# Optimization experiments

Hardware: AMD Instinct MI355X
Metric: run time of the kernel (lower is better)

The kernel has to match this reference:

```python
import jax, jax.numpy as jnp
import numpy as np

EPS = 1e-6      # eps used in token2map / map2token weight normalization
LN_EPS = 1e-5   # torch nn.LayerNorm default


def layernorm(x, w, b):
    m = jnp.mean(x, axis=-1, keepdims=True)
    xc = x - m
    v = jnp.mean(xc * xc, axis=-1, keepdims=True)
    return xc * jax.lax.rsqrt(v + LN_EPS) * w + b


def grid_index(H_init, W_init, H, W):
    # nearest-neighbor map: flattened feature-map index for each init-grid cell
    r = (jnp.arange(H_init) * H) // H_init
    c = (jnp.arange(W_init) * W) // W_init
    return (r[:, None] * W + c[None, :]).reshape(-1)  # [N_init]


def token2map(x, idx_token, H, W, H_init, W_init):
    # tokens [B,N,C] -> feature map [B,H,W,C] via weighted scatter-mean
    B, N, C = x.shape
    idx_hw = grid_index(H_init, W_init, H, W)                    # [N_init]
    counts = jnp.zeros((H * W,), x.dtype).at[idx_hw].add(1.0)    # identical across batch
    w = (1.0 / (counts + EPS))[idx_hw]                           # [N_init]
    src = jnp.take_along_axis(x, idx_token[..., None], axis=1)   # [B,N_init,C]
    out = jnp.zeros((B, H * W, C), x.dtype).at[:, idx_hw, :].add(src * w[None, :, None])
    return out.reshape(B, H, W, C)


def map2token(fmap, idx_token, N, H_init, W_init):
    # feature map [B,H,W,C] -> tokens [B,N,C]: mean of member grid cells per token
    B, H, W, C = fmap.shape
    idx_hw = grid_index(H_init, W_init, H, W)
    bidx = jnp.arange(B)[:, None]
    counts = jnp.zeros((B, N), fmap.dtype).at[bidx, idx_token].add(1.0)
    wt = jnp.take_along_axis(1.0 / (counts + EPS), idx_token, axis=1)  # [B,N_init]
    src = fmap.reshape(B, H * W, C)[:, idx_hw, :]                      # [B,N_init,C]
    return jnp.zeros((B, N, C), fmap.dtype).at[bidx, idx_token].add(src * wt[..., None])


def _forward(x, token_score, idx_token,
             norm1_w, norm1_b, q_w, q_b, kv_w, kv_b, sr_w, sr_b, srn_w, srn_b,
             proj_w, proj_b, norm2_w, norm2_b, fc1_w, fc1_b, skip_w, dw_w, dw_b,
             fc2_w, fc2_b, H, W, H_init, W_init, token_num, num_heads):
    B, N, C = x.shape
    d = C // num_heads
    scale = d ** -0.5
    sr = 2  # sr_ratio

    xn = layernorm(x, norm1_w, norm1_b)  # q_dict['x'] = norm1(x); kv_dict is q_dict

    # ---- TCFormerDynamicAttention ----
    q = (xn @ q_w + q_b).reshape(B, N, num_heads, d).transpose(0, 2, 1, 3)  # [B,h,N,d]
    tmp = jnp.concatenate([xn, token_score], axis=-1)            # [B,N,C+1]
    tmp_map = token2map(tmp, idx_token, H, W, H_init, W_init)    # [B,H,W,C+1]
    kv_map, conf_map = tmp_map[..., :C], tmp_map[..., C]
    kv = jax.lax.conv_general_dilated(kv_map, sr_w, (sr, sr), 'VALID',
        dimension_numbers=('NHWC', 'HWIO', 'NHWC')) + sr_b       # sr conv, stride 2
    M = (H // sr) * (W // sr)
    kv = layernorm(kv.reshape(B, M, C), srn_w, srn_b)
    conf = conf_map.reshape(B, H // sr, sr, W // sr, sr).mean(axis=(2, 4)).reshape(B, M)

    kv = (kv @ kv_w + kv_b).reshape(B, M, 2, num_heads, d)
    k = kv[:, :, 0].transpose(0, 2, 1, 3)                        # [B,h,M,d]
    v = kv[:, :, 1].transpose(0, 2, 1, 3)
    attn = jnp.einsum('bhnd,bhmd->bhnm', q * scale, k) + conf[:, None, None, :]
    attn = jax.nn.softmax(attn, axis=-1)
    a = jnp.einsum('bhnm,bhmd->bhnd', attn, v).transpose(0, 2, 1, 3).reshape(B, N, C)
    x = x + (a @ proj_w + proj_b)

    # ---- TCMLP ----
    h = layernorm(x, norm2_w, norm2_b) @ fc1_w + fc1_b           # [B,N,H1]
    hmap = token2map(h, idx_token, H, W, H_init, W_init)         # [B,H,W,H1]
    hmap = jax.lax.conv_general_dilated(hmap, dw_w, (1, 1), ((1, 1), (1, 1)),
        dimension_numbers=('NHWC', 'HWIO', 'NHWC'),
        feature_group_count=h.shape[-1]) + dw_b                  # depthwise 3x3
    hc = h * skip_w + map2token(hmap, idx_token, N, H_init, W_init)  # skip = dw 1x1 conv1d
    hc = jax.nn.gelu(hc, approximate=False)
    return x + (hc @ fc2_w + fc2_b)


def setup_inputs() -> dict:
    B, N, C, H1 = 8, 1568, 256, 1024
    H = W = 56
    H_init = W_init = 112
    key = jax.random.key(0)
    ks = jax.random.split(key, 16)
    r = lambda i, shape, s=0.02: jax.random.normal(ks[i], shape, jnp.float32) * s
    return {
        'x': jax.random.normal(ks[0], (B, N, C), jnp.float32),
        'token_score': jax.random.normal(ks[1], (B, N, 1), jnp.float32),
        'idx_token': jax.random.randint(ks[2], (B, H_init * W_init), 0, N),
        'norm1_w': jnp.ones((C,), jnp.float32), 'norm1_b': jnp.zeros((C,), jnp.float32),
        'q_w': r(3, (C, C)), 'q_b': jnp.zeros((C,), jnp.float32),
        'kv_w': r(4, (C, 2 * C)), 'kv_b': jnp.zeros((2 * C,), jnp.float32),
        'sr_w': r(5, (2, 2, C, C)), 'sr_b': jnp.zeros((C,), jnp.float32),
        'srn_w': jnp.ones((C,), jnp.float32), 'srn_b': jnp.zeros((C,), jnp.float32),
        'proj_w': r(6, (C, C)), 'proj_b': jnp.zeros((C,), jnp.float32),
        'norm2_w': jnp.ones((C,), jnp.float32), 'norm2_b': jnp.zeros((C,), jnp.float32),
        'fc1_w': r(7, (C, H1)), 'fc1_b': jnp.zeros((H1,), jnp.float32),
        'skip_w': 1.0 + r(8, (H1,), 0.1),
        'dw_w': r(9, (3, 3, 1, H1), 0.1), 'dw_b': jnp.zeros((H1,), jnp.float32),
        'fc2_w': r(10, (H1, C)), 'fc2_b': jnp.zeros((C,), jnp.float32),
        'H': H, 'W': W, 'H_init': H_init, 'W_init': W_init,
        'token_num': N, 'num_heads': 8,
    }


def reference(x, token_score, idx_token, norm1_w, norm1_b, q_w, q_b, kv_w, kv_b,
              sr_w, sr_b, srn_w, srn_b, proj_w, proj_b, norm2_w, norm2_b,
              fc1_w, fc1_b, skip_w, dw_w, dw_b, fc2_w, fc2_b,
              H, W, H_init, W_init, token_num, num_heads):
    return _forward(x, token_score, idx_token, norm1_w, norm1_b, q_w, q_b, kv_w, kv_b,
                    sr_w, sr_b, srn_w, srn_b, proj_w, proj_b, norm2_w, norm2_b,
                    fc1_w, fc1_b, skip_w, dw_w, dw_b, fc2_w, fc2_b,
                    H, W, H_init, W_init, token_num, num_heads)
```

## Files before the change

kernel.cpp:

```cpp
#include <hip/hip_runtime.h>
#include <math.h>

#define BB 8
#define NTOK 1568
#define CD 256
#define HIMG 56
#define WIMG 56
#define HWSZ 3136
#define HIG 112
#define WIG 112
#define NI 12544
#define MKV 784
#define MPAD 800
#define NHEADS 8
#define HEADD 32
#define HH1 1024
#define ROWS1 (BB*NTOK)
#define ROWSK (BB*MKV)
#define LOG2E 1.4426950408889634f

typedef unsigned short bfu;
typedef __attribute__((ext_vector_type(4))) unsigned short bf4;
typedef __attribute__((ext_vector_type(8))) unsigned short bf8;
typedef __attribute__((ext_vector_type(8))) short s8v;
typedef __attribute__((ext_vector_type(16))) float f16v;

__device__ inline float b2f(bfu u) { union { unsigned i; float f; } x; x.i = (unsigned)u << 16; return x.f; }
__device__ inline bfu f2b(float f) {
  union { float f; unsigned i; } x; x.f = f;
  unsigned r = x.i + 0x7fffu + ((x.i >> 16) & 1u);
  return (bfu)(r >> 16);
}
__device__ inline int get_isb(const unsigned* probe) { return probe[0] == 0x3F803F80u ? 1 : 0; }
__device__ inline float ldd(const void* p, size_t i, int isb) {
  return isb ? b2f(((const bfu*)p)[i]) : ((const float*)p)[i];
}
__device__ inline int xswz(int wg, int nwg) {
  return (nwg & 7) ? wg : (wg & 7) * (nwg >> 3) + (wg >> 3);
}

__global__ __launch_bounds__(256) void wtr_tile(const void* __restrict__ w0,
                                                const void* __restrict__ w1,
                                                const void* __restrict__ w2,
                                                const void* __restrict__ w3,
                                                const void* __restrict__ w4,
                                                const void* __restrict__ w5,
                                                const void* __restrict__ w6,
                                                const void* __restrict__ w7,
                                                bfu* __restrict__ wtb,
                                                const unsigned* __restrict__ probe) {
  int isb = get_isb(probe);
  int bid = blockIdx.x, tid = threadIdx.x;
  if (bid >= 1024) {
    int idx = (bid - 1024) * 256 + tid;
    if (idx < 9216) wtb[1048576 + idx] = f2b(ldd(w6, idx, isb));
    else            wtb[1048576 + idx] = f2b(ldd(w7, idx - 9216, isb));
    return;
  }
  const void* W; int K, N; bfu* Wt; int tloc;
  if (bid < 64)       { W = w0; K = 256;  N = 256;  Wt = wtb;          tloc = bid; }
  else if (bid < 320) { W = w1; K = 1024; N = 256;  Wt = wtb + 65536;  tloc = bid - 64; }
  else if (bid < 448) { W = w2; K = 256;  N = 512;  Wt = wtb + 327680; tloc = bid - 320; }
  else if (bid < 512) { W = w3; K = 256;  N = 256;  Wt = wtb + 458752; tloc = bid - 448; }
  else if (bid < 768) { W = w4; K = 256;  N = 1024; Wt = wtb + 524288; tloc = bid - 512; }
  else                { W = w5; K = 1024; N = 256;  Wt = wtb + 786432; tloc = bid - 768; }
  int ntn = N >> 5;
  int tn = tloc % ntn, tk = tloc / ntn;
  int n0 = tn * 32, k0 = tk * 32;
  __shared__ float s[32][33];
  int tx = tid & 31, ty = tid >> 5;
#pragma unroll
  for (int i = 0; i < 4; i++) {
    int k = ty + 8 * i;
    s[k][tx] = ldd(W, (size_t)(k0 + k) * N + n0 + tx, isb);
  }
  __syncthreads();
#pragma unroll
  for (int i = 0; i < 4; i++) {
    int n = ty + 8 * i;
    Wt[(size_t)(n0 + n) * K + k0 + tx] = f2b(s[tx][n]);
  }
}

__global__ __launch_bounds__(256) void ln_kernel(const void* __restrict__ in, int inmode,
                                                 const void* __restrict__ w,
                                                 const void* __restrict__ bta,
                                                 bfu* __restrict__ out,
                                                 const unsigned* __restrict__ probe) {
  int isb = get_isb(probe);
  int im = (inmode == 2) ? isb : inmode;
  int blk = xswz(blockIdx.x, gridDim.x);
  int wv = threadIdx.x >> 6, lane = threadIdx.x & 63;
  int row = blk * 4 + wv;
  int c4 = lane * 4;
  float v[4];
  if (im) {
    bf4 t = *(const bf4*)((const bfu*)in + (size_t)row * CD + c4);
#pragma unroll
    for (int j = 0; j < 4; j++) v[j] = b2f(t[j]);
  } else {
    float4 t = *(const float4*)((const float*)in + (size_t)row * CD + c4);
    v[0] = t.x; v[1] = t.y; v[2] = t.z; v[3] = t.w;
  }
  float s1 = v[0] + v[1] + v[2] + v[3];
  float s2 = v[0] * v[0] + v[1] * v[1] + v[2] * v[2] + v[3] * v[3];
#pragma unroll
  for (int off = 1; off < 64; off <<= 1) {
    s1 += __shfl_xor(s1, off);
    s2 += __shfl_xor(s2, off);
  }
  float m = s1 * (1.0f / CD);
  float inv = rsqrtf(s2 * (1.0f / CD) - m * m + 1e-5f);
  bf4 ov;
#pragma unroll
  for (int j = 0; j < 4; j++)
    ov[j] = f2b((v[j] - m) * inv * ldd(w, c4 + j, isb) + ldd(bta, c4 + j, isb));
  *(bf4*)(out + (size_t)row * CD + c4) = ov;
}

__global__ __launch_bounds__(256) void rgemm(const bfu* __restrict__ A,
                                             const bfu* __restrict__ Bt,
                                             const void* __restrict__ bias,
                                             const void* __restrict__ resid, int rmode,
                                             void* __restrict__ Cc, int cmode,
                                             void* __restrict__ aux,
                                             int K, int Ncols,
                                             const unsigned* __restrict__ probe) {
  int isb = get_isb(probe);
  int rm = (rmode == 1) ? (isb ? 3 : 2) : rmode;
  int cm = (cmode == 2) ? (isb ? 0 : 1) : cmode;
  int nbx = Ncols >> 6;
  int id = xswz(blockIdx.x, gridDim.x);
  int bx = id % nbx, by = id / nbx;
  int w = threadIdx.x >> 6, lane = threadIdx.x & 63;
  int l31 = lane & 31, hi = lane >> 5;
  int m0 = by * 128 + w * 32;
  int c0 = bx * 64;
  const bfu* pa  = A  + (size_t)(m0 + l31) * K + hi * 8;
  const bfu* pb0 = Bt + (size_t)(c0 + l31) * K + hi * 8;
  const bfu* pb1 = Bt + (size_t)(c0 + 32 + l31) * K + hi * 8;
  f16v acc0, acc1;
#pragma unroll
  for (int r = 0; r < 16; r++) { acc0[r] = 0.f; acc1[r] = 0.f; }
  s8v aA  = *(const s8v*)(pa),       b0A = *(const s8v*)(pb0),      b1A = *(const s8v*)(pb1);
  s8v aB  = *(const s8v*)(pa + 16),  b0B = *(const s8v*)(pb0 + 16), b1B = *(const s8v*)(pb1 + 16);
  for (int k0 = 32; k0 <= K; k0 += 32) {
    s8v caA = aA, cb0A = b0A, cb1A = b1A, caB = aB, cb0B = b0B, cb1B = b1B;
    if (k0 < K) {
      aA  = *(const s8v*)(pa + k0);       b0A = *(const s8v*)(pb0 + k0);      b1A = *(const s8v*)(pb1 + k0);
      aB  = *(const s8v*)(pa + k0 + 16);  b0B = *(const s8v*)(pb0 + k0 + 16); b1B = *(const s8v*)(pb1 + k0 + 16);
    }
    __builtin_amdgcn_s_setprio(1);
    acc0 = __builtin_amdgcn_mfma_f32_32x32x16_bf16(caA, cb0A, acc0, 0, 0, 0);
    acc1 = __builtin_amdgcn_mfma_f32_32x32x16_bf16(caA, cb1A, acc1, 0, 0, 0);
    acc0 = __builtin_amdgcn_mfma_f32_32x32x16_bf16(caB, cb0B, acc0, 0, 0, 0);
    acc1 = __builtin_amdgcn_mfma_f32_32x32x16_bf16(caB, cb1B, acc1, 0, 0, 0);
    __builtin_amdgcn_s_setprio(0);
  }
  float bw0 = ldd(bias, c0 + l31, isb);
  float bw1 = ldd(bias, c0 + 32 + l31, isb);
#pragma unroll
  for (int r = 0; r < 16; r++) {
    int row = m0 + (r & 3) + 8 * (r >> 2) + 4 * hi;
    size_t base0 = (size_t)row * Ncols + c0 + l31;
    size_t base1 = base0 + 32;
    float v0 = acc0[r] + bw0;
    float v1 = acc1[r] + bw1;
    if (rm == 2) { v0 += ((const float*)resid)[base0]; v1 += ((const float*)resid)[base1]; }
    else if (rm == 3) { v0 += b2f(((const bfu*)resid)[base0]); v1 += b2f(((const bfu*)resid)[base1]); }
    if (cm == 0) { ((bfu*)Cc)[base0] = f2b(v0); ((bfu*)Cc)[base1] = f2b(v1); }
    else if (cm == 1) { ((float*)Cc)[base0] = v0; ((float*)Cc)[base1] = v1; }
    else {
      int bb = row / MKV, mm = row - bb * MKV;
      int col0c = c0 + l31;
      if (col0c < 256) ((bfu*)Cc)[base0] = f2b(v0);
      else ((bfu*)aux)[((size_t)(bb * 256) + (col0c - 256)) * MPAD + mm] = f2b(v0);
      int col1c = col0c + 32;
      if (col1c < 256) ((bfu*)Cc)[base1] = f2b(v1);
      else ((bfu*)aux)[((size_t)(bb * 256) + (col1c - 256)) * MPAD + mm] = f2b(v1);
    }
  }
}

__global__ __launch_bounds__(256) void akv_kernel(const bfu* __restrict__ xn,
                                                  const void* __restrict__ tscore,
                                                  const int* __restrict__ idx_token,
                                                  bfu* __restrict__ Akv,
                                                  float* __restrict__ conf,
                                                  const unsigned* __restrict__ probe) {
  int isb = get_isb(probe);
  int blk = xswz(blockIdx.x, gridDim.x), tid = threadIdx.x;
  int b = blk / MKV, m = blk % MKV;
  int i2 = m / 28, j2 = m % 28;
  __shared__ int nn[16];
  __shared__ float cacc[16];
  if (tid < 16) {
    int a = (tid >> 3) & 1, kb = (tid >> 2) & 1, di = (tid >> 1) & 1, dj = tid & 1;
    int ti = 4 * i2 + 2 * a + di, tj = 4 * j2 + 2 * kb + dj;
    int n = idx_token[b * NI + ti * WIG + tj];
    nn[tid] = n;
    cacc[tid] = ldd(tscore, b * NTOK + n, isb);
  }
  __syncthreads();
  const float w4 = 1.0f / (4.0f + 1e-6f);
  int g = tid >> 6, c4 = (tid & 63) * 4;
  bf4 a0 = *(const bf4*)(xn + (size_t)(b * NTOK + nn[g * 4 + 0]) * CD + c4);
  bf4 a1 = *(const bf4*)(xn + (size_t)(b * NTOK + nn[g * 4 + 1]) * CD + c4);
  bf4 a2 = *(const bf4*)(xn + (size_t)(b * NTOK + nn[g * 4 + 2]) * CD + c4);
  bf4 a3 = *(const bf4*)(xn + (size_t)(b * NTOK + nn[g * 4 + 3]) * CD + c4);
  bf4 rv;
#pragma unroll
  for (int j = 0; j < 4; j++)
    rv[j] = f2b(w4 * (b2f(a0[j]) + b2f(a1[j]) + b2f(a2[j]) + b2f(a3[j])));
  *(bf4*)(Akv + (size_t)blk * 1024 + g * CD + c4) = rv;
  if (tid == 0) {
    float s = 0.f;
    for (int k = 0; k < 16; k++) s += cacc[k];
    conf[b * MPAD + m] = 0.25f * w4 * s * 5.656854249492381f;
  }
}

__global__ __launch_bounds__(256) void pad_kernel(bfu* __restrict__ vt, float* __restrict__ conf) {
  int t = blockIdx.x * 256 + threadIdx.x;
  int b = t / 4096, rem = t % 4096;
  int d = rem / 16, m = MKV + (rem % 16);
  vt[((size_t)(b * 256 + d)) * MPAD + m] = 0;
  if (t < 128) conf[(t / 16) * MPAD + MKV + (t % 16)] = -1e30f;
}

__global__ __launch_bounds__(256) void attn_kernel(const bfu* __restrict__ qb,
                                                   const bfu* __restrict__ kv,
                                                   const bfu* __restrict__ vt,
                                                   const float* __restrict__ conf,
                                                   bfu* __restrict__ out) {
  __shared__ float sdata[4][64][34];
  int tid = threadIdx.x;
  int w = tid >> 6, lane = tid & 63;
  int l31 = lane & 31, hi = lane >> 5;
  int blk = xswz(blockIdx.x, gridDim.x);
  int qt = blk % 25, tt = blk / 25;
  int hh = tt & 7, b = tt >> 3;
  int n0 = qt * 64;
  int two = (qt < 24);
  const bfu* qrow1 = qb + (size_t)(b * NTOK + n0 + l31) * CD + hh * HEADD + hi * 8;
  s8v qfA1 = *(const s8v*)(qrow1);
  s8v qfB1 = *(const s8v*)(qrow1 + 16);
  s8v qfA2 = {0, 0, 0, 0, 0, 0, 0, 0}, qfB2 = qfA2;
  if (two) {
    const bfu* qrow2 = qrow1 + (size_t)32 * CD;
    qfA2 = *(const s8v*)(qrow2);
    qfB2 = *(const s8v*)(qrow2 + 16);
  }
  const float scale = 0.17677669529663689f * LOG2E;
  const bfu* kbase = kv + hh * HEADD + hi * 8;
  const bfu* vbase = vt + ((size_t)(b * 256 + hh * HEADD + l31)) * MPAD + hi * 8;
  const float* cbase = conf + b * MPAD + 4 * hi;
  f16v oc1, oc2;
#pragma unroll
  for (int r = 0; r < 16; r++) { oc1[r] = 0.f; oc2[r] = 0.f; }
  float lr1 = 0.f, lr2 = 0.f;
  int w32 = w * 32;
  const bfu* kp0 = kbase + (size_t)(b * MKV + w32 + l31) * 512;
  s8v kfA = *(const s8v*)(kp0);
  s8v kfB = *(const s8v*)(kp0 + 16);
  s8v vfA = *(const s8v*)(vbase + w32);
  s8v vfB = *(const s8v*)(vbase + w32 + 16);
  float4 cf0 = *(const float4*)(cbase + w32);
  float4 cf1 = *(const float4*)(cbase + w32 + 8);
  float4 cf2 = *(const float4*)(cbase + w32 + 16);
  float4 cf3 = *(const float4*)(cbase + w32 + 24);
  for (int m0 = w32; m0 < MPAD; m0 += 128) {
    s8v ckA = kfA, ckB = kfB, cvA = vfA, cvB = vfB;
    float4 d0 = cf0, d1 = cf1, d2 = cf2, d3 = cf3;
    int m1 = m0 + 128;
    if (m1 < MPAD) {
      int mA = m1 + l31; if (mA > MKV - 1) mA = MKV - 1;
      const bfu* kp = kbase + (size_t)(b * MKV + mA) * 512;
      kfA = *(const s8v*)(kp);
      kfB = *(const s8v*)(kp + 16);
      vfA = *(const s8v*)(vbase + m1);
      vfB = *(const s8v*)(vbase + m1 + 16);
      cf0 = *(const float4*)(cbase + m1);
      cf1 = *(const float4*)(cbase + m1 + 8);
      cf2 = *(const float4*)(cbase + m1 + 16);
      cf3 = *(const float4*)(cbase + m1 + 24);
    }
    f16v cseed;
    cseed[0] = d0.x; cseed[1] = d0.y; cseed[2] = d0.z; cseed[3] = d0.w;
    cseed[4] = d1.x; cseed[5] = d1.y; cseed[6] = d1.z; cseed[7] = d1.w;
    cseed[8] = d2.x; cseed[9] = d2.y; cseed[10] = d2.z; cseed[11] = d2.w;
    cseed[12] = d3.x; cseed[13] = d3.y; cseed[14] = d3.z; cseed[15] = d3.w;
    __builtin_amdgcn_s_setprio(1);
    f16v c = __builtin_amdgcn_mfma_f32_32x32x16_bf16(ckA, qfA1, cseed, 0, 0, 0);
    c = __builtin_amdgcn_mfma_f32_32x32x16_bf16(ckB, qfB1, c, 0, 0, 0);
    __builtin_amdgcn_s_setprio(0);
    {
      float p[16], ps0 = 0.f, ps1 = 0.f, ps2 = 0.f, ps3 = 0.f;
#pragma unroll
      for (int r = 0; r < 16; r++) {
        p[r] = __builtin_amdgcn_exp2f(c[r] * scale);
        if ((r & 3) == 0) ps0 += p[r];
        else if ((r & 3) == 1) ps1 += p[r];
        else if ((r & 3) == 2) ps2 += p[r];
        else ps3 += p[r];
      }
      lr1 += (ps0 + ps1) + (ps2 + ps3);
      unsigned Z[8];
#pragma unroll
      for (int a2 = 0; a2 < 8; a2++)
        asm("v_cvt_pk_bf16_f32 %0, %1, %2" : "=v"(Z[a2]) : "v"(p[2 * a2]), "v"(p[2 * a2 + 1]));
      asm("v_permlane32_swap_b32 %0, %1" : "+v"(Z[0]), "+v"(Z[2]));
      asm("v_permlane32_swap_b32 %0, %1" : "+v"(Z[1]), "+v"(Z[3]));
      asm("v_permlane32_swap_b32 %0, %1" : "+v"(Z[4]), "+v"(Z[6]));
      asm("v_permlane32_swap_b32 %0, %1" : "+v"(Z[5]), "+v"(Z[7]));
      union { unsigned u[4]; s8v v; } B1, B2;
      B1.u[0] = Z[0]; B1.u[1] = Z[1]; B1.u[2] = Z[2]; B1.u[3] = Z[3];
      B2.u[0] = Z[4]; B2.u[1] = Z[5]; B2.u[2] = Z[6]; B2.u[3] = Z[7];
      __builtin_amdgcn_s_setprio(1);
      oc1 = __builtin_amdgcn_mfma_f32_32x32x16_bf16(cvA, B1.v, oc1, 0, 0, 0);
      oc1 = __builtin_amdgcn_mfma_f32_32x32x16_bf16(cvB, B2.v, oc1, 0, 0, 0);
      __builtin_amdgcn_s_setprio(0);
    }
    if (two) {
      __builtin_amdgcn_s_setprio(1);
      f16v c2 = __builtin_amdgcn_mfma_f32_32x32x16_bf16(ckA, qfA2, cseed, 0, 0, 0);
      c2 = __builtin_amdgcn_mfma_f32_32x32x16_bf16(ckB, qfB2, c2, 0, 0, 0);
      __builtin_amdgcn_s_setprio(0);
      float p[16], ps0 = 0.f, ps1 = 0.f, ps2 = 0.f, ps3 = 0.f;
#pragma unroll
      for (int r = 0; r < 16; r++) {
        p[r] = __builtin_amdgcn_exp2f(c2[r] * scale);
        if ((r & 3) == 0) ps0 += p[r];
        else if ((r & 3) == 1) ps1 += p[r];
        else if ((r & 3) == 2) ps2 += p[r];
        else ps3 += p[r];
      }
      lr2 += (ps0 + ps1) + (ps2 + ps3);
      unsigned Z[8];
#pragma unroll
      for (int a2 = 0; a2 < 8; a2++)
        asm("v_cvt_pk_bf16_f32 %0, %1, %2" : "=v"(Z[a2]) : "v"(p[2 * a2]), "v"(p[2 * a2 + 1]));
      asm("v_permlane32_swap_b32 %0, %1" : "+v"(Z[0]), "+v"(Z[2]));
      asm("v_permlane32_swap_b32 %0, %1" : "+v"(Z[1]), "+v"(Z[3]));
      asm("v_permlane32_swap_b32 %0, %1" : "+v"(Z[4]), "+v"(Z[6]));
      asm("v_permlane32_swap_b32 %0, %1" : "+v"(Z[5]), "+v"(Z[7]));
      union { unsigned u[4]; s8v v; } B1, B2;
      B1.u[0] = Z[0]; B1.u[1] = Z[1]; B1.u[2] = Z[2]; B1.u[3] = Z[3];
      B2.u[0] = Z[4]; B2.u[1] = Z[5]; B2.u[2] = Z[6]; B2.u[3] = Z[7];
      __builtin_amdgcn_s_setprio(1);
      oc2 = __builtin_amdgcn_mfma_f32_32x32x16_bf16(cvA, B1.v, oc2, 0, 0, 0);
      oc2 = __builtin_amdgcn_mfma_f32_32x32x16_bf16(cvB, B2.v, oc2, 0, 0, 0);
      __builtin_amdgcn_s_setprio(0);
    }
  }
#pragma unroll
  for (int r = 0; r < 16; r++) { sdata[w][lane][r] = oc1[r]; sdata[w][lane][17 + r] = oc2[r]; }
  sdata[w][lane][16] = lr1;
  sdata[w][lane][33] = lr2;
  __syncthreads();
  if (w == 0 || (w == 1 && two)) {
    int base = w * 17;
    float s[17];
#pragma unroll
    for (int r = 0; r < 17; r++)
      s[r] = sdata[0][lane][base + r] + sdata[1][lane][base + r] +
             sdata[2][lane][base + r] + sdata[3][lane][base + r];
    float l = s[16];
    l += __shfl_xor(l, 32);
    float inv = 1.0f / l;
    bfu* op = out + (size_t)(b * NTOK + n0 + w * 32 + l31) * CD + hh * HEADD + 4 * hi;
#pragma unroll
    for (int g = 0; g < 4; g++) {
      bf4 o;
#pragma unroll
      for (int u = 0; u < 4; u++) o[u] = f2b(s[4 * g + u] * inv);
      *(bf4*)(op + 8 * g) = o;
    }
  }
}

__global__ __launch_bounds__(128) void hmap_kernel(const bfu* __restrict__ h,
                                                   const int* __restrict__ idx_token,
                                                   bfu* __restrict__ hmap) {
  int blk = xswz(blockIdx.x, gridDim.x), tid = threadIdx.x;
  int b = blk / HWSZ, cell = blk % HWSZ;
  int i = cell / WIMG, j = cell % WIMG;
  __shared__ int nn[4];
  if (tid < 4) {
    int di = tid >> 1, dj = tid & 1;
    nn[tid] = idx_token[b * NI + (2 * i + di) * WIG + (2 * j + dj)];
  }
  __syncthreads();
  const float w4 = 1.0f / (4.0f + 1e-6f);
  int c8 = tid * 8;
  bf8 a0 = *(const bf8*)(h + (size_t)(b * NTOK + nn[0]) * HH1 + c8);
  bf8 a1 = *(const bf8*)(h + (size_t)(b * NTOK + nn[1]) * HH1 + c8);
  bf8 a2 = *(const bf8*)(h + (size_t)(b * NTOK + nn[2]) * HH1 + c8);
  bf8 a3 = *(const bf8*)(h + (size_t)(b * NTOK + nn[3]) * HH1 + c8);
  bf8 rv;
#pragma unroll
  for (int j2 = 0; j2 < 8; j2++)
    rv[j2] = f2b(w4 * (b2f(a0[j2]) + b2f(a1[j2]) + b2f(a2[j2]) + b2f(a3[j2])));
  *(bf8*)(hmap + (size_t)blk * HH1 + c8) = rv;
}

__global__ __launch_bounds__(256) void dw_kernel(const bfu* __restrict__ hmap,
                                                 const bfu* __restrict__ dwt,
                                                 const bfu* __restrict__ dbt,
                                                 bfu* __restrict__ dwout) {
  int blk = xswz(blockIdx.x, gridDim.x);
  int j4 = blk % 14; int rem = blk / 14;
  int i = rem % HIMG; int b = rem / HIMG;
  int tid = threadIdx.x;
  int c4 = tid * 4;
  int j0 = j4 * 4;
  float wf[9][4];
#pragma unroll
  for (int k = 0; k < 9; k++) {
    bf4 wv = *(const bf4*)(dwt + k * HH1 + c4);
#pragma unroll
    for (int u = 0; u < 4; u++) wf[k][u] = b2f(wv[u]);
  }
  bf4 bias = *(const bf4*)(dbt + c4);
  float bi[4];
#pragma unroll
  for (int u = 0; u < 4; u++) bi[u] = b2f(bias[u]);
  bf4 tp[3][6];
  const size_t bbase = (size_t)b * HWSZ;
#pragma unroll
  for (int r = 0; r < 3; r++) {
    int yy = i - 1 + r;
    bool rowok = (unsigned)yy < (unsigned)HIMG;
#pragma unroll
    for (int cc = 0; cc < 6; cc++) {
      int xx = j0 - 1 + cc;
      bf4 v = {0, 0, 0, 0};
      if (rowok && (unsigned)xx < (unsigned)WIMG)
        v = *(const bf4*)(hmap + (bbase + yy * WIMG + xx) * HH1 + c4);
      tp[r][cc] = v;
    }
  }
#pragma unroll
  for (int j = 0; j < 4; j++) {
    float acc[4] = {bi[0], bi[1], bi[2], bi[3]};
#pragma unroll
    for (int r = 0; r < 3; r++)
#pragma unroll
      for (int kx = 0; kx < 3; kx++) {
        bf4 hv = tp[r][j + kx];
#pragma unroll
        for (int u = 0; u < 4; u++) acc[u] += b2f(hv[u]) * wf[r * 3 + kx][u];
      }
    bf4 ov;
#pragma unroll
    for (int u = 0; u < 4; u++) ov[u] = f2b(acc[u]);
    *(bf4*)(dwout + (bbase + i * WIMG + j0 + j) * HH1 + c4) = ov;
  }
}

__global__ void zero_int(int* p) { p[blockIdx.x * 256 + threadIdx.x] = 0; }
__global__ void count_kernel(const int* __restrict__ idx, int* __restrict__ cnt) {
  int t = xswz(blockIdx.x, gridDim.x) * 256 + threadIdx.x;
  int b = t / NI;
  atomicAdd(&cnt[b * NTOK + idx[t]], 1);
}
__global__ __launch_bounds__(256) void scan_kernel(const int* __restrict__ cnt, int* __restrict__ offs) {
  int b = blockIdx.x, tid = threadIdx.x;
  __shared__ int s[NTOK];
  for (int i = tid; i < NTOK; i += 256) s[i] = cnt[b * NTOK + i];
  __syncthreads();
  for (int st = 1; st < NTOK; st <<= 1) {
    int vals[7]; int k = 0;
    for (int i = tid; i < NTOK; i += 256, k++) vals[k] = (i >= st) ? s[i - st] : 0;
    __syncthreads();
    k = 0;
    for (int i = tid; i < NTOK; i += 256, k++) s[i] += vals[k];
    __syncthreads();
  }
  for (int i = tid; i < NTOK; i += 256) offs[b * NTOK + i] = (i > 0) ? s[i - 1] : 0;
}
__global__ void fill_kernel(const int* __restrict__ idx, const int* __restrict__ offs,
                            int* __restrict__ cursor, int* __restrict__ tlist) {
  int t = xswz(blockIdx.x, gridDim.x) * 256 + threadIdx.x;
  int b = t / NI, tt = t % NI;
  int n = idx[t];
  int p = atomicAdd(&cursor[b * NTOK + n], 1);
  tlist[b * NI + offs[b * NTOK + n] + p] = tt;
}

__global__ __launch_bounds__(128) void m2t_kernel(const bfu* __restrict__ h,
                                                  const bfu* __restrict__ dwout,
                                                  const int* __restrict__ cnt,
                                                  const int* __restrict__ offs,
                                                  const int* __restrict__ tlist,
                                                  const void* __restrict__ skipw,
                                                  bfu* __restrict__ hc,
                                                  const unsigned* __restrict__ probe) {
  int isb = get_isb(probe);
  int blk = xswz(blockIdx.x, gridDim.x), tid = threadIdx.x;
  int b = blk / NTOK, n = blk % NTOK;
  int c = cnt[b * NTOK + n];
  int o0 = offs[b * NTOK + n];
  float inv = 1.0f / ((float)c + 1e-6f);
  int c8 = tid * 8;
  float a[8] = {};
  for (int k = 0; k < c; k++) {
    int tt = tlist[b * NI + o0 + k];
    int ti = tt / WIG, tj = tt % WIG;
    int cell = (ti >> 1) * WIMG + (tj >> 1);
    bf8 dv = *(const bf8*)(dwout + ((size_t)b * HWSZ + cell) * HH1 + c8);
#pragma unroll
    for (int j2 = 0; j2 < 8; j2++) a[j2] += b2f(dv[j2]);
  }
  bf8 hv = *(const bf8*)(h + (size_t)blk * HH1 + c8);
  bf8 ov;
  const float is2 = 0.70710678118654752f;
#pragma unroll
  for (int j2 = 0; j2 < 8; j2++) {
    float r = b2f(hv[j2]) * ldd(skipw, c8 + j2, isb) + a[j2] * inv;
    r = 0.5f * r * (1.0f + erff(r * is2));
    ov[j2] = f2b(r);
  }
  *(bf8*)(hc + (size_t)blk * HH1 + c8) = ov;
}

extern "C" void kernel_launch(void* const* d_in, const int* in_sizes, int n_in,
                              void* d_out, int out_size, void* d_ws, size_t ws_size,
                              hipStream_t stream) {
  const void* x        = d_in[0];
  const void* tscore   = d_in[1];
  const int*  idx_tok  = (const int*)d_in[2];
  const void* norm1_w  = d_in[3];
  const void* norm1_b  = d_in[4];
  const void* q_w      = d_in[5];
  const void* q_b      = d_in[6];
  const void* kv_w     = d_in[7];
  const void* kv_b     = d_in[8];
  const void* sr_w     = d_in[9];
  const void* sr_b     = d_in[10];
  const void* srn_w    = d_in[11];
  const void* srn_b    = d_in[12];
  const void* proj_w   = d_in[13];
  const void* proj_b   = d_in[14];
  const void* norm2_w  = d_in[15];
  const void* norm2_b  = d_in[16];
  const void* fc1_w    = d_in[17];
  const void* fc1_b    = d_in[18];
  const void* skip_w   = d_in[19];
  const void* dw_w     = d_in[20];
  const void* dw_b     = d_in[21];
  const void* fc2_w    = d_in[22];
  const void* fc2_b    = d_in[23];
  const unsigned* probe = (const unsigned*)d_in[3];

  float* ws = (float*)d_ws;
  size_t o = 0;
  float* x2 = ws + o;          o += (size_t)ROWS1 * CD;
  float* hR = ws + o;          o += (size_t)ROWS1 * HH1 / 2;
  float* mR = ws + o;          o += (size_t)BB * HWSZ * HH1 / 2;
  float* dR = ws + o;          o += (size_t)BB * HWSZ * HH1 / 2;
  int* ibase = (int*)(ws + o); o += (size_t)(3 * ROWS1 + BB * NI);
  bfu* wtb   = (bfu*)(ws + o); o += 529408;
  bfu* vtb   = (bfu*)(ws + o);

  bfu* Akv   = (bfu*)hR;
  bfu* kvc   = (bfu*)(hR + (size_t)ROWSK * 1024 / 2);
  bfu* h     = (bfu*)hR;
  bfu* qbuf  = (bfu*)mR;
  bfu* kvout = (bfu*)(mR + (size_t)ROWS1 * CD / 2);
  float* conf  = mR + (size_t)ROWS1 * CD / 2 + (size_t)ROWSK * 512 / 2;
  bfu* hmap  = (bfu*)mR;
  bfu* hc    = (bfu*)mR;
  bfu* xn    = (bfu*)dR;
  bfu* dwout = (bfu*)dR;
  int* counts = ibase;
  int* cursor = ibase + ROWS1;
  int* offs   = ibase + 2 * ROWS1;
  int* tlist  = ibase + 3 * ROWS1;
  bfu* q_wt    = wtb;
  bfu* sr_wt   = wtb + 65536;
  bfu* kv_wt   = wtb + 327680;
  bfu* proj_wt = wtb + 458752;
  bfu* fc1_wt  = wtb + 524288;
  bfu* fc2_wt  = wtb + 786432;
  bfu* dwt     = wtb + 1048576;
  bfu* dbt     = wtb + 1057792;

  wtr_tile<<<1064, 256, 0, stream>>>(q_w, sr_w, kv_w, proj_w, fc1_w, fc2_w, dw_w, dw_b, wtb, probe);
  pad_kernel<<<128, 256, 0, stream>>>(vtb, conf);

  ln_kernel<<<ROWS1 / 4, 256, 0, stream>>>(x, 2, norm1_w, norm1_b, xn, probe);
  rgemm<<<392, 256, 0, stream>>>(xn, q_wt, q_b, nullptr, 0, qbuf, 0, nullptr, 256, 256, probe);
  akv_kernel<<<ROWSK, 256, 0, stream>>>(xn, tscore, idx_tok, Akv, conf, probe);
  rgemm<<<196, 256, 0, stream>>>(Akv, sr_wt, sr_b, nullptr, 0, kvc, 0, nullptr, 1024, 256, probe);
  ln_kernel<<<ROWSK / 4, 256, 0, stream>>>(kvc, 1, srn_w, srn_b, kvc, probe);
  rgemm<<<392, 256, 0, stream>>>(kvc, kv_wt, kv_b, nullptr, 0, kvout, 3, vtb, 256, 512, probe);
  attn_kernel<<<BB * NHEADS * 25, 256, 0, stream>>>(qbuf, kvout, vtb, conf, xn);
  rgemm<<<392, 256, 0, stream>>>(xn, proj_wt, proj_b, x, 1, x2, 1, nullptr, 256, 256, probe);
  ln_kernel<<<ROWS1 / 4, 256, 0, stream>>>(x2, 0, norm2_w, norm2_b, xn, probe);
  rgemm<<<1568, 256, 0, stream>>>(xn, fc1_wt, fc1_b, nullptr, 0, h, 0, nullptr, 256, 1024, probe);
  hmap_kernel<<<BB * HWSZ, 128, 0, stream>>>(h, idx_tok, hmap);
  dw_kernel<<<BB * HIMG * 14, 256, 0, stream>>>(hmap, dwt, dbt, dwout);
  zero_int<<<(2 * ROWS1) / 256, 256, 0, stream>>>(counts);
  count_kernel<<<(BB * NI) / 256, 256, 0, stream>>>(idx_tok, counts);
  scan_kernel<<<BB, 256, 0, stream>>>(counts, offs);
  fill_kernel<<<(BB * NI) / 256, 256, 0, stream>>>(idx_tok, offs, cursor, tlist);
  m2t_kernel<<<ROWS1, 128, 0, stream>>>(h, dwout, counts, offs, tlist, skip_w, hc, probe);
  rgemm<<<392, 256, 0, stream>>>(hc, fc2_wt, fc2_b, x2, 2, d_out, 2, nullptr, 1024, 256, probe);
}
```

Before: 482.6 us.

## Replace register-direct GEMM with LDS double-buffered 64x64 tile GEMM

Replaces the GEMM, which loaded A and B fragments straight from global memory into registers with 32x32 MFMA, by a kernel that stages 64x64 A/B tiles in padded, double-buffered LDS and computes with 16x16x32 MFMA. Tiles shrink from 128x64 to 64x64, doubling the grid for every GEMM launch. The goal is to reuse B rows across waves through shared memory and to spread work over more blocks. In exchange it adds a __syncthreads per K step, LDS traffic, and more total global reads of the weight matrix because tiles are smaller.

```diff
diff --git a/kernel.cpp b/kernel.cpp
--- a/kernel.cpp
+++ b/kernel.cpp
@@ -23,6 +23,7 @@
 typedef __attribute__((ext_vector_type(4))) unsigned short bf4;
 typedef __attribute__((ext_vector_type(8))) unsigned short bf8;
 typedef __attribute__((ext_vector_type(8))) short s8v;
+typedef __attribute__((ext_vector_type(4))) float f4v;
 typedef __attribute__((ext_vector_type(16))) float f16v;
 
 __device__ inline float b2f(bfu u) { union { unsigned i; float f; } x; x.i = (unsigned)u << 16; return x.f; }
@@ -118,66 +119,79 @@
   *(bf4*)(out + (size_t)row * CD + c4) = ov;
 }
 
-__global__ __launch_bounds__(256) void rgemm(const bfu* __restrict__ A,
-                                             const bfu* __restrict__ Bt,
-                                             const void* __restrict__ bias,
-                                             const void* __restrict__ resid, int rmode,
-                                             void* __restrict__ Cc, int cmode,
-                                             void* __restrict__ aux,
-                                             int K, int Ncols,
-                                             const unsigned* __restrict__ probe) {
+__global__ __launch_bounds__(256) void gemm2ph(const bfu* __restrict__ A,
+                                               const bfu* __restrict__ Bt,
+                                               const void* __restrict__ bias,
+                                               const void* __restrict__ resid, int rmode,
+                                               void* __restrict__ Cc, int cmode,
+                                               void* __restrict__ aux,
+                                               int K, int Ncols,
+                                               const unsigned* __restrict__ probe) {
   int isb = get_isb(probe);
   int rm = (rmode == 1) ? (isb ? 3 : 2) : rmode;
   int cm = (cmode == 2) ? (isb ? 0 : 1) : cmode;
+  __shared__ bfu As[2][64][40];
+  __shared__ bfu Bs[2][64][40];
+  int t = threadIdx.x;
   int nbx = Ncols >> 6;
   int id = xswz(blockIdx.x, gridDim.x);
-  int bx = id % nbx, by = id / nbx;
-  int w = threadIdx.x >> 6, lane = threadIdx.x & 63;
-  int l31 = lane & 31, hi = lane >> 5;
-  int m0 = by * 128 + w * 32;
-  int c0 = bx * 64;
-  const bfu* pa  = A  + (size_t)(m0 + l31) * K + hi * 8;
-  const bfu* pb0 = Bt + (size_t)(c0 + l31) * K + hi * 8;
-  const bfu* pb1 = Bt + (size_t)(c0 + 32 + l31) * K + hi * 8;
-  f16v acc0, acc1;
-#pragma unroll
-  for (int r = 0; r < 16; r++) { acc0[r] = 0.f; acc1[r] = 0.f; }
-  s8v aA  = *(const s8v*)(pa),       b0A = *(const s8v*)(pb0),      b1A = *(const s8v*)(pb1);
-  s8v aB  = *(const s8v*)(pa + 16),  b0B = *(const s8v*)(pb0 + 16), b1B = *(const s8v*)(pb1 + 16);
+  int row0 = (id / nbx) * 64, col0 = (id % nbx) * 64;
+  int sr = t >> 2, sc = (t & 3) * 8;
+  int w = t >> 6, lane = t & 63;
+  int li = lane & 15, q = lane >> 4;
+  int wm = w * 16;
+  const bfu* pa = A + (size_t)(row0 + sr) * K + sc;
+  const bfu* pb = Bt + (size_t)(col0 + sr) * K + sc;
+  f4v zz = {0.f, 0.f, 0.f, 0.f};
+  f4v acc[4];
+#pragma unroll
+  for (int ni = 0; ni < 4; ni++) acc[ni] = zz;
+  s8v la = *(const s8v*)(pa);
+  s8v lb = *(const s8v*)(pb);
+  int cur = 0;
   for (int k0 = 32; k0 <= K; k0 += 32) {
-    s8v caA = aA, cb0A = b0A, cb1A = b1A, caB = aB, cb0B = b0B, cb1B = b1B;
+    *(s8v*)(&As[cur][sr][sc]) = la;
+    *(s8v*)(&Bs[cur][sr][sc]) = lb;
+    __syncthreads();
     if (k0 < K) {
-      aA  = *(const s8v*)(pa + k0);       b0A = *(const s8v*)(pb0 + k0);      b1A = *(const s8v*)(pb1 + k0);
-      aB  = *(const s8v*)(pa + k0 + 16);  b0B = *(const s8v*)(pb0 + k0 + 16); b1B = *(const s8v*)(pb1 + k0 + 16);
+      la = *(const s8v*)(pa + k0);
+      lb = *(const s8v*)(pb + k0);
     }
+    s8v af  = *(const s8v*)(&As[cur][wm + li][q * 8]);
+    s8v bf0 = *(const s8v*)(&Bs[cur][li][q * 8]);
+    s8v bf1 = *(const s8v*)(&Bs[cur][16 + li][q * 8]);
+    s8v bf2 = *(const s8v*)(&Bs[cur][32 + li][q * 8]);
+    s8v bf3 = *(const s8v*)(&Bs[cur][48 + li][q * 8]);
     __builtin_amdgcn_s_setprio(1);
-    acc0 = __builtin_amdgcn_mfma_f32_32x32x16_bf16(caA, cb0A, acc0, 0, 0, 0);
-    acc1 = __builtin_amdgcn_mfma_f32_32x32x16_bf16(caA, cb1A, acc1, 0, 0, 0);
-    acc0 = __builtin_amdgcn_mfma_f32_32x32x16_bf16(caB, cb0B, acc0, 0, 0, 0);
-    acc1 = __builtin_amdgcn_mfma_f32_32x32x16_bf16(caB, cb1B, acc1, 0, 0, 0);
+    acc[0] = __builtin_amdgcn_mfma_f32_16x16x32_bf16(af, bf0, acc[0], 0, 0, 0);
+    acc[1] = __builtin_amdgcn_mfma_f32_16x16x32_bf16(af, bf1, acc[1], 0, 0, 0);
+    acc[2] = __builtin_amdgcn_mfma_f32_16x16x32_bf16(af, bf2, acc[2], 0, 0, 0);
+    acc[3] = __builtin_amdgcn_mfma_f32_16x16x32_bf16(af, bf3, acc[3], 0, 0, 0);
     __builtin_amdgcn_s_setprio(0);
-  }
-  float bw0 = ldd(bias, c0 + l31, isb);
-  float bw1 = ldd(bias, c0 + 32 + l31, isb);
-#pragma unroll
-  for (int r = 0; r < 16; r++) {
-    int row = m0 + (r & 3) + 8 * (r >> 2) + 4 * hi;
-    size_t base0 = (size_t)row * Ncols + c0 + l31;
-    size_t base1 = base0 + 32;
-    float v0 = acc0[r] + bw0;
-    float v1 = acc1[r] + bw1;
-    if (rm == 2) { v0 += ((const float*)resid)[base0]; v1 += ((const float*)resid)[base1]; }
-    else if (rm == 3) { v0 += b2f(((const bfu*)resid)[base0]); v1 += b2f(((const bfu*)resid)[base1]); }
-    if (cm == 0) { ((bfu*)Cc)[base0] = f2b(v0); ((bfu*)Cc)[base1] = f2b(v1); }
-    else if (cm == 1) { ((float*)Cc)[base0] = v0; ((float*)Cc)[base1] = v1; }
-    else {
-      int bb = row / MKV, mm = row - bb * MKV;
-      int col0c = c0 + l31;
-      if (col0c < 256) ((bfu*)Cc)[base0] = f2b(v0);
-      else ((bfu*)aux)[((size_t)(bb * 256) + (col0c - 256)) * MPAD + mm] = f2b(v0);
-      int col1c = col0c + 32;
-      if (col1c < 256) ((bfu*)Cc)[base1] = f2b(v1);
-      else ((bfu*)aux)[((size_t)(bb * 256) + (col1c - 256)) * MPAD + mm] = f2b(v1);
+    cur ^= 1;
+  }
+  float bw[4];
+#pragma unroll
+  for (int ni = 0; ni < 4; ni++) bw[ni] = ldd(bias, col0 + ni * 16 + li, isb);
+#pragma unroll
+  for (int ni = 0; ni < 4; ni++) {
+    int col = col0 + ni * 16 + li;
+#pragma unroll
+    for (int r = 0; r < 4; r++) {
+      int row = row0 + wm + q * 4 + r;
+      size_t base = (size_t)row * Ncols + col;
+      float v = acc[ni][r] + bw[ni];
+      if (rm == 2) v += ((const float*)resid)[base];
+      else if (rm == 3) v += b2f(((const bfu*)resid)[base]);
+      if (cm == 0) ((bfu*)Cc)[base] = f2b(v);
+      else if (cm == 1) ((float*)Cc)[base] = v;
+      else {
+        if (col < 256) ((bfu*)Cc)[base] = f2b(v);
+        else {
+          int bb = row / MKV, mm = row - bb * MKV;
+          ((bfu*)aux)[((size_t)(bb * 256) + (col - 256)) * MPAD + mm] = f2b(v);
+        }
+      }
     }
   }
 }
@@ -590,15 +604,15 @@
   pad_kernel<<<128, 256, 0, stream>>>(vtb, conf);
 
   ln_kernel<<<ROWS1 / 4, 256, 0, stream>>>(x, 2, norm1_w, norm1_b, xn, probe);
-  rgemm<<<392, 256, 0, stream>>>(xn, q_wt, q_b, nullptr, 0, qbuf, 0, nullptr, 256, 256, probe);
+  gemm2ph<<<784, 256, 0, stream>>>(xn, q_wt, q_b, nullptr, 0, qbuf, 0, nullptr, 256, 256, probe);
   akv_kernel<<<ROWSK, 256, 0, stream>>>(xn, tscore, idx_tok, Akv, conf, probe);
-  rgemm<<<196, 256, 0, stream>>>(Akv, sr_wt, sr_b, nullptr, 0, kvc, 0, nullptr, 1024, 256, probe);
+  gemm2ph<<<392, 256, 0, stream>>>(Akv, sr_wt, sr_b, nullptr, 0, kvc, 0, nullptr, 1024, 256, probe);
   ln_kernel<<<ROWSK / 4, 256, 0, stream>>>(kvc, 1, srn_w, srn_b, kvc, probe);
-  rgemm<<<392, 256, 0, stream>>>(kvc, kv_wt, kv_b, nullptr, 0, kvout, 3, vtb, 256, 512, probe);
+  gemm2ph<<<784, 256, 0, stream>>>(kvc, kv_wt, kv_b, nullptr, 0, kvout, 3, vtb, 256, 512, probe);
   attn_kernel<<<BB * NHEADS * 25, 256, 0, stream>>>(qbuf, kvout, vtb, conf, xn);
-  rgemm<<<392, 256, 0, stream>>>(xn, proj_wt, proj_b, x, 1, x2, 1, nullptr, 256, 256, probe);
+  gemm2ph<<<784, 256, 0, stream>>>(xn, proj_wt, proj_b, x, 1, x2, 1, nullptr, 256, 256, probe);
   ln_kernel<<<ROWS1 / 4, 256, 0, stream>>>(x2, 0, norm2_w, norm2_b, xn, probe);
-  rgemm<<<1568, 256, 0, stream>>>(xn, fc1_wt, fc1_b, nullptr, 0, h, 0, nullptr, 256, 1024, probe);
+  gemm2ph<<<3136, 256, 0, stream>>>(xn, fc1_wt, fc1_b, nullptr, 0, h, 0, nullptr, 256, 1024, probe);
   hmap_kernel<<<BB * HWSZ, 128, 0, stream>>>(h, idx_tok, hmap);
   dw_kernel<<<BB * HIMG * 14, 256, 0, stream>>>(hmap, dwt, dbt, dwout);
   zero_int<<<(2 * ROWS1) / 256, 256, 0, stream>>>(counts);
@@ -606,5 +620,5 @@
   scan_kernel<<<BB, 256, 0, stream>>>(counts, offs);
   fill_kernel<<<(BB * NI) / 256, 256, 0, stream>>>(idx_tok, offs, cursor, tlist);
   m2t_kernel<<<ROWS1, 128, 0, stream>>>(h, dwout, counts, offs, tlist, skip_w, hc, probe);
-  rgemm<<<392, 256, 0, stream>>>(hc, fc2_wt, fc2_b, x2, 2, d_out, 2, nullptr, 1024, 256, probe);
-}
+  gemm2ph<<<784, 256, 0, stream>>>(hc, fc2_wt, fc2_b, x2, 2, d_out, 2, nullptr, 1024, 256, probe);
+}
```

After: 408.5 us. 1.18x faster.
